# Optimization experiments

Hardware: AMD Instinct MI355X
Metric: run time of the kernel (lower is better)

The kernel has to match this reference:

```python
import jax, jax.numpy as jnp
import numpy as np

N_NODES = 50000
N_EDGES = 800000
D = 128


def setup_inputs() -> dict:
    key = jax.random.key(0)
    ks = jax.random.split(key, 8)
    s = 1.0 / np.sqrt(D)
    return {
        "x": jax.random.normal(ks[0], (N_NODES, D), dtype=jnp.float32),
        "edge_index": jax.random.randint(ks[1], (2, N_EDGES), 0, N_NODES, dtype=jnp.int32),
        "W0l": jax.random.normal(ks[2], (D, D), dtype=jnp.float32) * s,
        "b0l": jnp.zeros((D,), dtype=jnp.float32),
        "W0r": jax.random.normal(ks[3], (D, D), dtype=jnp.float32) * s,
        "W1l": jax.random.normal(ks[4], (D, D), dtype=jnp.float32) * s,
        "b1l": jnp.zeros((D,), dtype=jnp.float32),
        "W1r": jax.random.normal(ks[5], (D, D), dtype=jnp.float32) * s,
    }


def reference(x, edge_index, W0l, b0l, W0r, W1l, b1l, W1r):
    # Encoder(conv='sage', num_layers=2), eval mode (dropout = identity).
    src = edge_index[0]  # x_j gathered from source nodes
    dst = edge_index[1]  # aggregated at target nodes
    # in-degree for mean aggregation; isolated nodes get 0 aggregate (PyG mean)
    deg = jax.ops.segment_sum(jnp.ones_like(dst, dtype=x.dtype), dst, num_segments=N_NODES)
    inv_deg = jnp.where(deg > 0, 1.0 / jnp.maximum(deg, 1.0), 0.0)[:, None]

    def sage(h, Wl, bl, Wr):
        m = h @ Wl + bl                                        # lin_l
        agg = jax.ops.segment_sum(m[src], dst, num_segments=N_NODES) * inv_deg  # mean aggr
        return agg + h @ Wr                                    # + lin_r skip

    h = jax.nn.relu(sage(x, W0l, b0l, W0r))   # layer 0 + relu
    return sage(h, W1l, b1l, W1r)             # final layer
```

## Files before the change

kernel.cpp:

```cpp
#include <hip/hip_runtime.h>

#define N_NODES 50000
#define N_EDGES 800000
#define D 128
#define NBLK ((N_NODES + 255) / 256)
#define EPB 4096
#define CAP 8192
#define PCAP 8192

typedef __bf16 bf16x8 __attribute__((ext_vector_type(8)));
typedef short s16x8 __attribute__((ext_vector_type(8)));
typedef float f32x4 __attribute__((ext_vector_type(4)));
typedef float f32x2 __attribute__((ext_vector_type(2)));
typedef unsigned short u16;
typedef unsigned int u32;
typedef unsigned char u8;
typedef u32 u32x2 __attribute__((ext_vector_type(2)));
typedef u32 u32x4 __attribute__((ext_vector_type(4)));

__device__ inline u16 f32_to_bf16(float f) {
    u32 u = __builtin_bit_cast(u32, f);
    u += 0x7fffu + ((u >> 16) & 1u);
    return (u16)(u >> 16);
}
__device__ inline float bf16_lo(u32 v) { return __builtin_bit_cast(float, v << 16); }
__device__ inline float bf16_hi(u32 v) { return __builtin_bit_cast(float, v & 0xffff0000u); }

__device__ inline f32x4 mfma16(s16x8 a, s16x8 b, f32x4 c) {
    return __builtin_amdgcn_mfma_f32_16x16x32_bf16(
        __builtin_bit_cast(bf16x8, a), __builtin_bit_cast(bf16x8, b), c, 0, 0, 0);
}

#define CAST_BLOCKS ((N_NODES * 16) / 256)
#define STAGE_BLOCKS ((N_EDGES + EPB - 1) / EPB)

__global__ __launch_bounds__(256) void prep_stage(
    const float* __restrict__ x, u16* __restrict__ xb, u16* __restrict__ hb,
    u8* __restrict__ xf8, u8* __restrict__ hf8,
    const float* __restrict__ W0l, const float* __restrict__ W0r,
    const float* __restrict__ W1l, const float* __restrict__ W1r,
    u16* __restrict__ Wp,
    const int* __restrict__ src, const int* __restrict__ dst,
    int* __restrict__ ccount, u32* __restrict__ staged) {
    __shared__ int hist[NBLK];
    __shared__ int base[NBLK];
    int t = threadIdx.x, b = blockIdx.x;
    if (b < CAST_BLOCKS) {
        int gid = b * 256 + t;
        const float* p = x + (size_t)gid * 8;
        f32x4 a = *(const f32x4*)p;
        f32x4 c = *(const f32x4*)(p + 4);
        u16 o[8];
#pragma unroll
        for (int j = 0; j < 4; j++) { o[j] = f32_to_bf16(a[j]); o[4 + j] = f32_to_bf16(c[j]); }
        *(s16x8*)(xb + (size_t)gid * 8) = *(const s16x8*)o;
        int p0 = __builtin_amdgcn_cvt_pk_fp8_f32(a.x, a.y, 0, false);
        int p1 = __builtin_amdgcn_cvt_pk_fp8_f32(a.z, a.w, 0, false);
        int p2 = __builtin_amdgcn_cvt_pk_fp8_f32(c.x, c.y, 0, false);
        int p3 = __builtin_amdgcn_cvt_pk_fp8_f32(c.z, c.w, 0, false);
        u32x2 w;
        w.x = (u32)(p0 & 0xffff) | ((u32)(p1 & 0xffff) << 16);
        w.y = (u32)(p2 & 0xffff) | ((u32)(p3 & 0xffff) << 16);
        *(u32x2*)(xf8 + (size_t)gid * 8) = w;
    } else if (b < CAST_BLOCKS + 32) {
        int gid = (b - CAST_BLOCKS) * 256 + t;
        int wsel = gid >> 11;
        int rem  = gid & 2047;
        int ct   = rem >> 8;
        int ks   = (rem >> 6) & 3;
        int lane = rem & 63;
        const float* W = (wsel == 0) ? W0l : (wsel == 1) ? W0r : (wsel == 2) ? W1l : W1r;
        int n  = ct * 16 + (lane & 15);
        int k0 = ks * 32 + (lane >> 4) * 8;
        u16 o[8];
#pragma unroll
        for (int j = 0; j < 8; j++) o[j] = f32_to_bf16(W[(k0 + j) * D + n]);
        u16* dp = Wp + wsel * 16384 + (size_t)((ct * 4 + ks) * 64 + lane) * 8;
        *(s16x8*)dp = *(const s16x8*)o;
    } else if (b < CAST_BLOCKS + 33) {
        if (t < 64)        ((u32*)(xb + (size_t)N_NODES * D))[t] = 0;
        else if (t < 128)  ((u32*)(hb + (size_t)N_NODES * D))[t - 64] = 0;
        else if (t < 160)  ((u32*)(xf8 + (size_t)N_NODES * D))[t - 128] = 0;
        else if (t < 192)  ((u32*)(hf8 + (size_t)N_NODES * D))[t - 160] = 0;
    } else {
        int sb = b - CAST_BLOCKS - 33;
        int bb = sb * EPB;
        if (t < NBLK) hist[t] = 0;
        __syncthreads();
        u32 pk[16]; int cb[16];
#pragma unroll
        for (int i = 0; i < 16; i++) {
            int e = bb + i * 256 + t;
            if (e < N_EDGES) {
                int sv = src[e], dv = dst[e];
                pk[i] = (u32)sv | ((u32)(dv & 255) << 16);
                cb[i] = dv >> 8;
                atomicAdd(&hist[cb[i]], 1);
            } else cb[i] = -1;
        }
        __syncthreads();
        if (t < NBLK) {
            int c = hist[t];
            if (c > 0) {
                int old = atomicAdd(&ccount[t], c);
                if (old > CAP - c) old = CAP - c;
                base[t] = t * CAP + old;
            }
            hist[t] = 0;
        }
        __syncthreads();
#pragma unroll
        for (int i = 0; i < 16; i++) {
            if (cb[i] >= 0) {
                int slot = atomicAdd(&hist[cb[i]], 1);
                staged[base[cb[i]] + slot] = pk[i];
            }
        }
    }
}

__global__ __launch_bounds__(256) void fine_kernel(const int* __restrict__ ccount,
                                                   const u32* __restrict__ staged,
                                                   u16* __restrict__ eidx,
                                                   u32* __restrict__ info,
                                                   float* __restrict__ inv) {
    __shared__ u32 sdata[CAP];
    __shared__ int hist[256];
    __shared__ int cursor[256];
    __shared__ int wsum[4];
    int t = threadIdx.x, cb = blockIdx.x;
    int lane = t & 63, wave = t >> 6;

    hist[t] = 0;
    __syncthreads();
    int c = ccount[cb];
    if (c > CAP) c = CAP;
    for (int i = t; i < c; i += 256) {
        u32 v = staged[cb * CAP + i];
        sdata[i] = v;
        atomicAdd(&hist[(v >> 16) & 255], 1);
    }
    __syncthreads();
    int d = hist[t];
    int pd = (d + 15) & ~15;
    int s = pd;
#pragma unroll
    for (int off = 1; off < 64; off <<= 1) {
        int u = __shfl_up(s, off, 64);
        if (lane >= off) s += u;
    }
    if (lane == 63) wsum[wave] = s;
    __syncthreads();
    int wadd = 0;
#pragma unroll
    for (int w = 0; w < 4; w++) if (w < wave) wadd += wsum[w];
    int gb = cb * PCAP + (s - pd + wadd);
    int node = cb * 256 + t;
    if (node < N_NODES) {
        info[node] = (u32)gb | ((u32)(pd >> 4) << 21);
        inv[node] = d > 0 ? 1.0f / (float)d : 0.0f;
    }
    cursor[t] = gb;
    __syncthreads();
    for (int i = t; i < c; i += 256) {
        u32 v = sdata[i];
        int pos = atomicAdd(&cursor[(v >> 16) & 255], 1);
        eidx[pos] = (u16)(v & 0xffffu);
    }
    for (int i = gb + d; i < gb + pd; i++) eidx[i] = (u16)N_NODES;
}

template <int RELU, int OUTF32>
__global__ __launch_bounds__(256) void fused_layer(
    const u16* __restrict__ A, const u8* __restrict__ AF8,
    const u16* __restrict__ WpR, const u16* __restrict__ WpL,
    const float* __restrict__ bias, const float* __restrict__ inv,
    const u32* __restrict__ info, const u16* __restrict__ eidx,
    u16* __restrict__ outb, u8* __restrict__ outf8, float* __restrict__ outf) {
    __shared__ char mlds[16 * 256];
    int wave = threadIdx.x >> 6, lane = threadIdx.x & 63;
    int rowbase = blockIdx.x * 16;
    int quad = lane >> 4, ql = lane & 15;

    int basek[4], rnds[4];
#pragma unroll
    for (int k = 0; k < 4; k++) {
        u32 ifo = info[rowbase + wave * 4 + k];
        basek[k] = (int)(ifo & 0x1FFFFFu);
        rnds[k]  = (int)(ifo >> 21);
    }
    int maxr = rnds[0];
#pragma unroll
    for (int k = 1; k < 4; k++) maxr = rnds[k] > maxr ? rnds[k] : maxr;

    float acc[4][8];
#pragma unroll
    for (int k = 0; k < 4; k++)
#pragma unroll
        for (int j = 0; j < 8; j++) acc[k][j] = 0.f;

#pragma unroll 1
    for (int r = 0; r < maxr; r++) {
        u32x2 g[4][4];
#pragma unroll
        for (int k = 0; k < 4; k++) {
            if (r < rnds[k]) {
                int i0 = basek[k] + r * 16 + quad;
                int s0 = eidx[i0], s1 = eidx[i0 + 4], s2 = eidx[i0 + 8], s3 = eidx[i0 + 12];
                g[k][0] = *(const u32x2*)(AF8 + (size_t)s0 * D + ql * 8);
                g[k][1] = *(const u32x2*)(AF8 + (size_t)s1 * D + ql * 8);
                g[k][2] = *(const u32x2*)(AF8 + (size_t)s2 * D + ql * 8);
                g[k][3] = *(const u32x2*)(AF8 + (size_t)s3 * D + ql * 8);
            }
        }
#pragma unroll
        for (int k = 0; k < 4; k++) {
            if (r < rnds[k]) {
#pragma unroll
                for (int j = 0; j < 4; j++) {
                    u32x2 v = g[k][j];
                    f32x2 f0 = __builtin_amdgcn_cvt_pk_f32_fp8((int)v.x, false);
                    f32x2 f1 = __builtin_amdgcn_cvt_pk_f32_fp8((int)v.x, true);
                    f32x2 f2 = __builtin_amdgcn_cvt_pk_f32_fp8((int)v.y, false);
                    f32x2 f3 = __builtin_amdgcn_cvt_pk_f32_fp8((int)v.y, true);
                    acc[k][0] += f0.x; acc[k][1] += f0.y;
                    acc[k][2] += f1.x; acc[k][3] += f1.y;
                    acc[k][4] += f2.x; acc[k][5] += f2.y;
                    acc[k][6] += f3.x; acc[k][7] += f3.y;
                }
            }
        }
    }

#pragma unroll
    for (int k = 0; k < 4; k++) {
#pragma unroll
        for (int j = 0; j < 8; j++) {
            acc[k][j] += __shfl_xor(acc[k][j], 16);
            acc[k][j] += __shfl_xor(acc[k][j], 32);
        }
        if (quad == 0) {
            int node = rowbase + wave * 4 + k;
            float iv = inv[node];
            u32x4 o;
            o.x = (u32)f32_to_bf16(acc[k][0] * iv) | ((u32)f32_to_bf16(acc[k][1] * iv) << 16);
            o.y = (u32)f32_to_bf16(acc[k][2] * iv) | ((u32)f32_to_bf16(acc[k][3] * iv) << 16);
            o.z = (u32)f32_to_bf16(acc[k][4] * iv) | ((u32)f32_to_bf16(acc[k][5] * iv) << 16);
            o.w = (u32)f32_to_bf16(acc[k][6] * iv) | ((u32)f32_to_bf16(acc[k][7] * iv) << 16);
            int lr = wave * 4 + k;
            *(u32x4*)(mlds + lr * 256 + ((ql ^ lr) & 15) * 16) = o;
        }
    }

    s16x8 bR[2][4], bL[2][4];
#pragma unroll
    for (int ct = 0; ct < 2; ct++) {
        int ctg = wave * 2 + ct;
#pragma unroll
        for (int ks = 0; ks < 4; ks++) {
            size_t off = (size_t)((ctg * 4 + ks) * 64 + lane) * 8;
            bR[ct][ks] = *(const s16x8*)(WpR + off);
            bL[ct][ks] = *(const s16x8*)(WpL + off);
        }
    }
    __syncthreads();

    f32x4 acc2[2];
    acc2[0] = (f32x4){0.f, 0.f, 0.f, 0.f};
    acc2[1] = (f32x4){0.f, 0.f, 0.f, 0.f};
#pragma unroll
    for (int ks = 0; ks < 4; ks++) {
        s16x8 a1 = *(const s16x8*)(A + (size_t)(rowbase + ql) * D + ks * 32 + quad * 8);
        s16x8 a2 = *(const s16x8*)(mlds + ql * 256 + (((ks * 4 + quad) ^ ql) & 15) * 16);
#pragma unroll
        for (int ct = 0; ct < 2; ct++) {
            acc2[ct] = mfma16(a1, bR[ct][ks], acc2[ct]);
            acc2[ct] = mfma16(a2, bL[ct][ks], acc2[ct]);
        }
    }

    float bv[2];
#pragma unroll
    for (int ct = 0; ct < 2; ct++) bv[ct] = bias[wave * 32 + ct * 16 + ql];

#pragma unroll
    for (int i = 0; i < 4; i++) {
        int row = rowbase + quad * 4 + i;
        float mask = inv[row] > 0.f ? 1.f : 0.f;
#pragma unroll
        for (int ct = 0; ct < 2; ct++) {
            int col = wave * 32 + ct * 16 + ql;
            float v = acc2[ct][i] + mask * bv[ct];
            if (RELU) v = v > 0.f ? v : 0.f;
            if (OUTF32) {
                outf[(size_t)row * D + col] = v;
            } else {
                outb[(size_t)row * D + col] = f32_to_bf16(v);
                int pk = __builtin_amdgcn_cvt_pk_fp8_f32(v, v, 0, false);
                outf8[(size_t)row * D + col] = (u8)(pk & 0xff);
            }
        }
    }
}

extern "C" void kernel_launch(void* const* d_in, const int* in_sizes, int n_in,
                              void* d_out, int out_size, void* d_ws, size_t ws_size,
                              hipStream_t stream) {
    const float* x    = (const float*)d_in[0];
    const int*   edge = (const int*)d_in[1];
    const int*   src  = edge;
    const int*   dstn = edge + N_EDGES;
    const float* W0l  = (const float*)d_in[2];
    const float* b0l  = (const float*)d_in[3];
    const float* W0r  = (const float*)d_in[4];
    const float* W1l  = (const float*)d_in[5];
    const float* b1l  = (const float*)d_in[6];
    const float* W1r  = (const float*)d_in[7];
    float* out = (float*)d_out;

    char* p = (char*)d_ws;
    auto alloc = [&](size_t nb) { char* r = p; p += (nb + 255) & ~(size_t)255; return r; };
    int*   ccount = (int*)alloc((size_t)NBLK * 4);
    u32*   info   = (u32*)alloc((size_t)N_NODES * 4);
    float* inv    = (float*)alloc((size_t)N_NODES * 4);
    u32*   staged = (u32*)alloc((size_t)NBLK * CAP * 4);
    u16*   eidx   = (u16*)alloc((size_t)NBLK * PCAP * 2);
    u16*   xb     = (u16*)alloc((size_t)(N_NODES + 1) * D * 2);
    u16*   hb     = (u16*)alloc((size_t)(N_NODES + 1) * D * 2);
    u8*    xf8    = (u8*)alloc((size_t)(N_NODES + 1) * D);
    u8*    hf8    = (u8*)alloc((size_t)(N_NODES + 1) * D);
    u16*   Wp     = (u16*)alloc((size_t)4 * 16384 * 2);

    hipMemsetAsync(ccount, 0, (size_t)NBLK * 4, stream);

    prep_stage<<<CAST_BLOCKS + 33 + STAGE_BLOCKS, 256, 0, stream>>>(
        x, xb, hb, xf8, hf8, W0l, W0r, W1l, W1r, Wp, src, dstn, ccount, staged);
    fine_kernel<<<NBLK, 256, 0, stream>>>(ccount, staged, eidx, info, inv);

    int fblocks = N_NODES / 16;
    const u16* WpL0 = Wp;
    const u16* WpR0 = Wp + 16384;
    const u16* WpL1 = Wp + 2 * 16384;
    const u16* WpR1 = Wp + 3 * 16384;
    fused_layer<1, 0><<<fblocks, 256, 0, stream>>>(xb, xf8, WpR0, WpL0, b0l, inv, info, eidx, hb, hf8, nullptr);
    fused_layer<0, 1><<<fblocks, 256, 0, stream>>>(hb, hf8, WpR1, WpL1, b1l, inv, info, eidx, nullptr, nullptr, out);
}
```

Baseline: 202.1 us.

## Use 8 waves per block with software-pipelined edge gather in fused layer

The fused SAGE layer now launches 512 threads (8 waves), so each wave aggregates 2 rows instead of 4 and owns one 16-column tile of the output GEMM. The gather loop is double-buffered: edge indices for round r+2 and fp8 feature rows for round r+1 are issued while round r is unpacked, and indices are read as a single u16x4 vector load. This aims to hide gather latency and raise parallelism per block. The cost is more registers for the two buffers and twice as many waves loading weight fragments, which may limit occupancy.

```diff
diff --git a/kernel.cpp b/kernel.cpp
--- a/kernel.cpp
+++ b/kernel.cpp
@@ -17,14 +17,13 @@
 typedef unsigned char u8;
 typedef u32 u32x2 __attribute__((ext_vector_type(2)));
 typedef u32 u32x4 __attribute__((ext_vector_type(4)));
+typedef u16 u16x4 __attribute__((ext_vector_type(4)));
 
 __device__ inline u16 f32_to_bf16(float f) {
     u32 u = __builtin_bit_cast(u32, f);
     u += 0x7fffu + ((u >> 16) & 1u);
     return (u16)(u >> 16);
 }
-__device__ inline float bf16_lo(u32 v) { return __builtin_bit_cast(float, v << 16); }
-__device__ inline float bf16_hi(u32 v) { return __builtin_bit_cast(float, v & 0xffff0000u); }
 
 __device__ inline f32x4 mfma16(s16x8 a, s16x8 b, f32x4 c) {
     return __builtin_amdgcn_mfma_f32_16x16x32_bf16(
@@ -170,8 +169,42 @@
     for (int i = gb + d; i < gb + pd; i++) eidx[i] = (u16)N_NODES;
 }
 
+__device__ inline void issue_e(u16x4 (&e)[2], const u16* __restrict__ eidx,
+                               const int (&basek)[2], const int (&rnds)[2],
+                               int quad, int rr) {
+#pragma unroll
+    for (int k = 0; k < 2; k++)
+        if (rr < rnds[k]) e[k] = *(const u16x4*)(eidx + basek[k] + rr * 16 + quad * 4);
+}
+__device__ inline void issue_g(u32x2 (&g)[2][4], const u16x4 (&e)[2],
+                               const u8* __restrict__ AF8, const int (&rnds)[2],
+                               int ql, int rr) {
+#pragma unroll
+    for (int k = 0; k < 2; k++)
+        if (rr < rnds[k]) {
+#pragma unroll
+            for (int j = 0; j < 4; j++)
+                g[k][j] = *(const u32x2*)(AF8 + (size_t)e[k][j] * D + ql * 8);
+        }
+}
+__device__ inline void unpack_acc(f32x2 (&acc)[2][4], const u32x2 (&g)[2][4],
+                                  const int (&rnds)[2], int rr) {
+#pragma unroll
+    for (int k = 0; k < 2; k++)
+        if (rr < rnds[k]) {
+#pragma unroll
+            for (int j = 0; j < 4; j++) {
+                u32x2 v = g[k][j];
+                acc[k][0] += __builtin_amdgcn_cvt_pk_f32_fp8((int)v.x, false);
+                acc[k][1] += __builtin_amdgcn_cvt_pk_f32_fp8((int)v.x, true);
+                acc[k][2] += __builtin_amdgcn_cvt_pk_f32_fp8((int)v.y, false);
+                acc[k][3] += __builtin_amdgcn_cvt_pk_f32_fp8((int)v.y, true);
+            }
+        }
+}
+
 template <int RELU, int OUTF32>
-__global__ __launch_bounds__(256) void fused_layer(
+__global__ __launch_bounds__(512) void fused_layer(
     const u16* __restrict__ A, const u8* __restrict__ AF8,
     const u16* __restrict__ WpR, const u16* __restrict__ WpL,
     const float* __restrict__ bias, const float* __restrict__ inv,
@@ -182,123 +215,96 @@
     int rowbase = blockIdx.x * 16;
     int quad = lane >> 4, ql = lane & 15;
 
-    int basek[4], rnds[4];
-#pragma unroll
-    for (int k = 0; k < 4; k++) {
-        u32 ifo = info[rowbase + wave * 4 + k];
+    int basek[2], rnds[2];
+#pragma unroll
+    for (int k = 0; k < 2; k++) {
+        u32 ifo = info[rowbase + wave * 2 + k];
         basek[k] = (int)(ifo & 0x1FFFFFu);
         rnds[k]  = (int)(ifo >> 21);
     }
-    int maxr = rnds[0];
-#pragma unroll
-    for (int k = 1; k < 4; k++) maxr = rnds[k] > maxr ? rnds[k] : maxr;
-
-    float acc[4][8];
-#pragma unroll
-    for (int k = 0; k < 4; k++)
-#pragma unroll
-        for (int j = 0; j < 8; j++) acc[k][j] = 0.f;
-
-#pragma unroll 1
-    for (int r = 0; r < maxr; r++) {
-        u32x2 g[4][4];
-#pragma unroll
-        for (int k = 0; k < 4; k++) {
-            if (r < rnds[k]) {
-                int i0 = basek[k] + r * 16 + quad;
-                int s0 = eidx[i0], s1 = eidx[i0 + 4], s2 = eidx[i0 + 8], s3 = eidx[i0 + 12];
-                g[k][0] = *(const u32x2*)(AF8 + (size_t)s0 * D + ql * 8);
-                g[k][1] = *(const u32x2*)(AF8 + (size_t)s1 * D + ql * 8);
-                g[k][2] = *(const u32x2*)(AF8 + (size_t)s2 * D + ql * 8);
-                g[k][3] = *(const u32x2*)(AF8 + (size_t)s3 * D + ql * 8);
-            }
-        }
-#pragma unroll
-        for (int k = 0; k < 4; k++) {
-            if (r < rnds[k]) {
-#pragma unroll
-                for (int j = 0; j < 4; j++) {
-                    u32x2 v = g[k][j];
-                    f32x2 f0 = __builtin_amdgcn_cvt_pk_f32_fp8((int)v.x, false);
-                    f32x2 f1 = __builtin_amdgcn_cvt_pk_f32_fp8((int)v.x, true);
-                    f32x2 f2 = __builtin_amdgcn_cvt_pk_f32_fp8((int)v.y, false);
-                    f32x2 f3 = __builtin_amdgcn_cvt_pk_f32_fp8((int)v.y, true);
-                    acc[k][0] += f0.x; acc[k][1] += f0.y;
-                    acc[k][2] += f1.x; acc[k][3] += f1.y;
-                    acc[k][4] += f2.x; acc[k][5] += f2.y;
-                    acc[k][6] += f3.x; acc[k][7] += f3.y;
-                }
-            }
-        }
-    }
-
-#pragma unroll
-    for (int k = 0; k < 4; k++) {
+    int maxr = rnds[0] > rnds[1] ? rnds[0] : rnds[1];
+
+    f32x2 acc[2][4];
+#pragma unroll
+    for (int k = 0; k < 2; k++)
+#pragma unroll
+        for (int e = 0; e < 4; e++) acc[k][e] = (f32x2){0.f, 0.f};
+
+    if (maxr > 0) {
+        u16x4 eA[2], eB[2];
+        u32x2 gA[2][4], gB[2][4];
+        issue_e(eA, eidx, basek, rnds, quad, 0);
+        issue_g(gA, eA, AF8, rnds, ql, 0);
+        if (maxr > 1) issue_e(eB, eidx, basek, rnds, quad, 1);
+        int r = 0;
+        while (true) {
+            if (r + 1 < maxr) issue_g(gB, eB, AF8, rnds, ql, r + 1);
+            if (r + 2 < maxr) issue_e(eA, eidx, basek, rnds, quad, r + 2);
+            unpack_acc(acc, gA, rnds, r);
+            if (++r >= maxr) break;
+            if (r + 1 < maxr) issue_g(gA, eA, AF8, rnds, ql, r + 1);
+            if (r + 2 < maxr) issue_e(eB, eidx, basek, rnds, quad, r + 2);
+            unpack_acc(acc, gB, rnds, r);
+            if (++r >= maxr) break;
+        }
+    }
+
+#pragma unroll
+    for (int k = 0; k < 2; k++) {
+        float v[8];
+#pragma unroll
+        for (int e = 0; e < 4; e++) { v[2 * e] = acc[k][e].x; v[2 * e + 1] = acc[k][e].y; }
 #pragma unroll
         for (int j = 0; j < 8; j++) {
-            acc[k][j] += __shfl_xor(acc[k][j], 16);
-            acc[k][j] += __shfl_xor(acc[k][j], 32);
+            v[j] += __shfl_xor(v[j], 16);
+            v[j] += __shfl_xor(v[j], 32);
         }
         if (quad == 0) {
-            int node = rowbase + wave * 4 + k;
+            int node = rowbase + wave * 2 + k;
             float iv = inv[node];
             u32x4 o;
-            o.x = (u32)f32_to_bf16(acc[k][0] * iv) | ((u32)f32_to_bf16(acc[k][1] * iv) << 16);
-            o.y = (u32)f32_to_bf16(acc[k][2] * iv) | ((u32)f32_to_bf16(acc[k][3] * iv) << 16);
-            o.z = (u32)f32_to_bf16(acc[k][4] * iv) | ((u32)f32_to_bf16(acc[k][5] * iv) << 16);
-            o.w = (u32)f32_to_bf16(acc[k][6] * iv) | ((u32)f32_to_bf16(acc[k][7] * iv) << 16);
-            int lr = wave * 4 + k;
+            o.x = (u32)f32_to_bf16(v[0] * iv) | ((u32)f32_to_bf16(v[1] * iv) << 16);
+            o.y = (u32)f32_to_bf16(v[2] * iv) | ((u32)f32_to_bf16(v[3] * iv) << 16);
+            o.z = (u32)f32_to_bf16(v[4] * iv) | ((u32)f32_to_bf16(v[5] * iv) << 16);
+            o.w = (u32)f32_to_bf16(v[6] * iv) | ((u32)f32_to_bf16(v[7] * iv) << 16);
+            int lr = wave * 2 + k;
             *(u32x4*)(mlds + lr * 256 + ((ql ^ lr) & 15) * 16) = o;
         }
     }
 
-    s16x8 bR[2][4], bL[2][4];
-#pragma unroll
-    for (int ct = 0; ct < 2; ct++) {
-        int ctg = wave * 2 + ct;
-#pragma unroll
-        for (int ks = 0; ks < 4; ks++) {
-            size_t off = (size_t)((ctg * 4 + ks) * 64 + lane) * 8;
-            bR[ct][ks] = *(const s16x8*)(WpR + off);
-            bL[ct][ks] = *(const s16x8*)(WpL + off);
-        }
-    }
-    __syncthreads();
-
-    f32x4 acc2[2];
-    acc2[0] = (f32x4){0.f, 0.f, 0.f, 0.f};
-    acc2[1] = (f32x4){0.f, 0.f, 0.f, 0.f};
+    s16x8 bR[4], bL[4];
+#pragma unroll
+    for (int ks = 0; ks < 4; ks++) {
+        size_t off = (size_t)((wave * 4 + ks) * 64 + lane) * 8;
+        bR[ks] = *(const s16x8*)(WpR + off);
+        bL[ks] = *(const s16x8*)(WpL + off);
+    }
+    __syncthreads();
+
+    f32x4 acc2 = (f32x4){0.f, 0.f, 0.f, 0.f};
 #pragma unroll
     for (int ks = 0; ks < 4; ks++) {
         s16x8 a1 = *(const s16x8*)(A + (size_t)(rowbase + ql) * D + ks * 32 + quad * 8);
         s16x8 a2 = *(const s16x8*)(mlds + ql * 256 + (((ks * 4 + quad) ^ ql) & 15) * 16);
-#pragma unroll
-        for (int ct = 0; ct < 2; ct++) {
-            acc2[ct] = mfma16(a1, bR[ct][ks], acc2[ct]);
-            acc2[ct] = mfma16(a2, bL[ct][ks], acc2[ct]);
-        }
-    }
-
-    float bv[2];
-#pragma unroll
-    for (int ct = 0; ct < 2; ct++) bv[ct] = bias[wave * 32 + ct * 16 + ql];
+        acc2 = mfma16(a1, bR[ks], acc2);
+        acc2 = mfma16(a2, bL[ks], acc2);
+    }
+
+    float bv = bias[wave * 16 + ql];
 
 #pragma unroll
     for (int i = 0; i < 4; i++) {
         int row = rowbase + quad * 4 + i;
         float mask = inv[row] > 0.f ? 1.f : 0.f;
-#pragma unroll
-        for (int ct = 0; ct < 2; ct++) {
-            int col = wave * 32 + ct * 16 + ql;
-            float v = acc2[ct][i] + mask * bv[ct];
-            if (RELU) v = v > 0.f ? v : 0.f;
-            if (OUTF32) {
-                outf[(size_t)row * D + col] = v;
-            } else {
-                outb[(size_t)row * D + col] = f32_to_bf16(v);
-                int pk = __builtin_amdgcn_cvt_pk_fp8_f32(v, v, 0, false);
-                outf8[(size_t)row * D + col] = (u8)(pk & 0xff);
-            }
+        int col = wave * 16 + ql;
+        float val = acc2[i] + mask * bv;
+        if (RELU) val = val > 0.f ? val : 0.f;
+        if (OUTF32) {
+            outf[(size_t)row * D + col] = val;
+        } else {
+            outb[(size_t)row * D + col] = f32_to_bf16(val);
+            int pk = __builtin_amdgcn_cvt_pk_fp8_f32(val, val, 0, false);
+            outf8[(size_t)row * D + col] = (u8)(pk & 0xff);
         }
     }
 }
@@ -342,6 +348,6 @@
     const u16* WpR0 = Wp + 16384;
     const u16* WpL1 = Wp + 2 * 16384;
     const u16* WpR1 = Wp + 3 * 16384;
-    fused_layer<1, 0><<<fblocks, 256, 0, stream>>>(xb, xf8, WpR0, WpL0, b0l, inv, info, eidx, hb, hf8, nullptr);
-    fused_layer<0, 1><<<fblocks, 256, 0, stream>>>(hb, hf8, WpR1, WpL1, b1l, inv, info, eidx, nullptr, nullptr, out);
-}
+    fused_layer<1, 0><<<fblocks, 512, 0, stream>>>(xb, xf8, WpR0, WpL0, b0l, inv, info, eidx, hb, hf8, nullptr);
+    fused_layer<0, 1><<<fblocks, 512, 0, stream>>>(hb, hf8, WpR1, WpL1, b1l, inv, info, eidx, nullptr, nullptr, out);
+}
```

Result: no change. 206.1 us (+2.0%).
